# Kernel tuning notes

Measured on AMD Instinct MI355X. Metric: run time of the kernel, lower is better.

## Reference

```python
import jax, jax.numpy as jnp
import numpy as np

OUT_FEATURES = 11008
IN_FEATURES = 4096
BLOCK_SIZE = 128
NUM_BLOCKS = IN_FEATURES // BLOCK_SIZE  # 32
M_TOKENS = 4096  # flattened batch*seq


def _pack_int4(q):
    # q: int8 values in [-8, 7], flattened; pack 2 nibbles per int8 (matches pack_int4_to_int8)
    flat = q.reshape(-1)
    u = (flat.astype(jnp.int32) + 8).astype(jnp.uint8)
    packed = (u[0::2] | (u[1::2] << 4)).astype(jnp.int8)
    return packed


def _unpack_int4(packed, shape):
    # matches unpack_int8_to_int4
    pu = packed.astype(jnp.uint8)
    lower = pu & 15
    upper = (pu >> 4) & 15
    un = jnp.stack([lower, upper], axis=1).reshape(-1)
    n = int(np.prod(shape))
    un = un[:n].astype(jnp.int8) - 8
    return un.reshape(shape)


def setup_inputs() -> dict:
    key = jax.random.key(0)
    k_x, k_w, k_b = jax.random.split(key, 3)
    x = jax.random.normal(k_x, (M_TOKENS, IN_FEATURES), dtype=jnp.float32)
    w = jax.random.normal(k_w, (OUT_FEATURES, IN_FEATURES), dtype=jnp.float32) * 0.02
    bias = jax.random.normal(k_b, (OUT_FEATURES,), dtype=jnp.float32) * 0.01
    # blockwise symmetric 4-bit quantization (matches _quantize_blockwise)
    wr = w.reshape(OUT_FEATURES, NUM_BLOCKS, BLOCK_SIZE).transpose(1, 2, 0)  # (nb, bs, out)
    max_val = jnp.max(jnp.abs(wr), axis=1, keepdims=True)  # (nb, 1, out)
    qmax = 7.0
    scale3 = jnp.clip(max_val / qmax, 1e-8, None)
    q = jnp.clip(jnp.round(wr / scale3), -8, 7).astype(jnp.int8)  # (nb, bs, out)
    scale = scale3.squeeze(1)  # (nb, out)
    packed_w = _pack_int4(q)
    return {"x": x, "packed_w": packed_w, "scale": scale, "bias": bias}


def reference(x, packed_w, scale, bias):
    # unpack int4 nibbles -> (num_blocks, block_size, out)
    q = _unpack_int4(packed_w, (NUM_BLOCKS, BLOCK_SIZE, OUT_FEATURES))
    # dequantize with per-(block, out-channel) scale
    w_deq = q.astype(jnp.float32) * scale[:, None, :]  # (nb, bs, out)
    # y = x @ W^T + b, with x blocked along the in dimension
    xb = x.reshape(x.shape[0], NUM_BLOCKS, BLOCK_SIZE)
    y = jnp.einsum('mnb,nbo->mo', xb, w_deq) + bias
    return y
```

## Files before the change

### kernel.cpp

```cpp
#include <hip/hip_runtime.h>
#include <hip/hip_bf16.h>
#include <stdint.h>

#define NOUT 11008
#define KIN  4096
#define MTOK 4096
#define PLD  5504
#define NSTEP 128
#define NTN 43
#define NTM 16
#define ACHUNK 16384
#define BCHUNK 16384
#define WSA_BYTES ((size_t)NTM * NSTEP * ACHUNK)
#define WSW_BYTES ((size_t)NTN * NSTEP * BCHUNK)

typedef short bf16x8 __attribute__((ext_vector_type(8)));
typedef float f32x4  __attribute__((ext_vector_type(4)));

typedef __attribute__((address_space(3))) uint8_t lds_u8_t;
typedef __attribute__((address_space(1))) const uint8_t glb_u8_t;

__device__ __forceinline__ uint32_t bfpack(float lo, float hi){
    __hip_bfloat16 a = __float2bfloat16(lo);
    __hip_bfloat16 b = __float2bfloat16(hi);
    uint16_t ua, ub;
    __builtin_memcpy(&ua, &a, 2);
    __builtin_memcpy(&ub, &b, 2);
    return (uint32_t)ua | ((uint32_t)ub << 16);
}

__device__ __forceinline__ int swzA(int r){ return ((r >> 1) & 3) << 4; }

__global__ __launch_bounds__(256)
void prepA(const float* __restrict__ x, uint8_t* __restrict__ wsA)
{
    int gid = blockIdx.x * 256 + threadIdx.x;
    int m  = gid >> 10;
    int k  = (gid & 1023) << 2;
    float4 v = *reinterpret_cast<const float4*>(x + (size_t)m * KIN + k);
    uint32_t lo = bfpack(v.x, v.y), hi = bfpack(v.z, v.w);
    int mt = m >> 8, ml = m & 255, t = k >> 5, kl = k & 31;
    size_t dst = (size_t)(mt * NSTEP + t) * ACHUNK + ml * 64 + ((kl * 2) ^ swzA(ml));
    *reinterpret_cast<uint2*>(wsA + dst) = make_uint2(lo, hi);
}

__global__ __launch_bounds__(256)
void prepW2(const int32_t* __restrict__ pw, const float* __restrict__ sc,
            uint8_t* __restrict__ wsW)
{
    const int t  = blockIdx.x;
    const int nt = blockIdx.y;
    const int c  = threadIdx.x;
    const int col = nt * 256 + c;
    const int np  = col >> 1;
    const uint32_t sh = (uint32_t)(col & 1) * 4;
    const int32_t* p = pw + (size_t)(t * 32) * PLD + np;
    const float s  = sc[(size_t)(t >> 2) * NOUT + col];
    const float m8 = -8.f * s;
    uint8_t* out = wsW + ((size_t)nt * NSTEP + t) * BCHUNK + c * 64;
#pragma unroll
    for (int k8 = 0; k8 < 4; ++k8) {
        uint32_t r[4];
#pragma unroll
        for (int kk = 0; kk < 4; ++kk) {
            uint32_t w0 = (uint32_t)p[(size_t)(k8 * 8 + kk * 2)     * PLD];
            uint32_t w1 = (uint32_t)p[(size_t)(k8 * 8 + kk * 2 + 1) * PLD];
            float f0 = fmaf((float)((w0 >> sh) & 15u), s, m8);
            float f1 = fmaf((float)((w1 >> sh) & 15u), s, m8);
            r[kk] = bfpack(f0, f1);
        }
        *reinterpret_cast<uint4*>(out + ((k8 * 16) ^ swzA(c))) = *reinterpret_cast<uint4*>(r);
    }
}

__global__ __launch_bounds__(512, 1)
void qlin_gemm8(const uint8_t* __restrict__ wsA, const uint8_t* __restrict__ wsW,
                const float* __restrict__ bias, float* __restrict__ y)
{
    __shared__ __align__(16) uint8_t ldsA[4][ACHUNK];
    __shared__ __align__(16) uint8_t ldsB[4][BCHUNK];

    const int tid  = threadIdx.x;
    const int lane = tid & 63;
    const int wid  = tid >> 6;
    const int wr = wid >> 2, wc = wid & 3;

    const int lb = (blockIdx.x & 7) * 86 + (blockIdx.x >> 3);
    const int mt = lb / NTN, nt = lb % NTN;
    const int m0 = mt * 256, n0 = nt * 256;

    const int cl = lane & 15;
    const int k8 = lane >> 4;

    int aOff[8];
#pragma unroll
    for (int i = 0; i < 8; ++i) {
        int ml = wr * 128 + i * 16 + cl;
        aOff[i] = ml * 64 + ((k8 * 16) ^ swzA(ml));
    }
    int bOff[4];
#pragma unroll
    for (int j = 0; j < 4; ++j) {
        int cc = wc * 64 + j * 16 + cl;
        bOff[j] = cc * 64 + ((k8 * 16) ^ swzA(cc));
    }

    const uint8_t* wsAbase = wsA + (size_t)mt * NSTEP * ACHUNK;
    const uint8_t* wsWbase = wsW + (size_t)nt * NSTEP * BCHUNK;

    f32x4 acc[8][4];
#pragma unroll
    for (int i = 0; i < 8; ++i)
#pragma unroll
        for (int j = 0; j < 4; ++j)
            acc[i][j] = (f32x4){0.f, 0.f, 0.f, 0.f};

    bf16x8 af[4], bfr[4];

#define STAGE_A(buf, t) do { \
    const uint8_t* g_ = wsAbase + (size_t)(t) * ACHUNK + tid * 16; \
    __builtin_amdgcn_global_load_lds((glb_u8_t*)(g_),        (lds_u8_t*)(&ldsA[buf][tid*16]),        16, 0, 0); \
    __builtin_amdgcn_global_load_lds((glb_u8_t*)(g_ + 8192), (lds_u8_t*)(&ldsA[buf][tid*16 + 8192]), 16, 0, 0); \
} while(0)

#define STAGE_B(buf, t) do { \
    const uint8_t* g_ = wsWbase + (size_t)(t) * BCHUNK + tid * 16; \
    __builtin_amdgcn_global_load_lds((glb_u8_t*)(g_),        (lds_u8_t*)(&ldsB[buf][tid*16]),        16, 0, 0); \
    __builtin_amdgcn_global_load_lds((glb_u8_t*)(g_ + 8192), (lds_u8_t*)(&ldsB[buf][tid*16 + 8192]), 16, 0, 0); \
} while(0)

#define BAR() do { \
    asm volatile("" ::: "memory"); \
    __builtin_amdgcn_s_barrier(); \
    asm volatile("" ::: "memory"); \
} while(0)

#define PHASE_ODD(cb, sb, st) do { \
    STAGE_A(sb, st); \
    _Pragma("unroll") \
    for (int i = 0; i < 4; ++i) \
        af[i] = *reinterpret_cast<const bf16x8*>(ldsA[cb] + aOff[i]); \
    _Pragma("unroll") \
    for (int j = 0; j < 4; ++j) \
        bfr[j] = *reinterpret_cast<const bf16x8*>(ldsB[cb] + bOff[j]); \
    BAR(); \
    asm volatile("s_waitcnt lgkmcnt(0)" ::: "memory"); \
    __builtin_amdgcn_sched_barrier(0); \
    __builtin_amdgcn_s_setprio(1); \
    _Pragma("unroll") \
    for (int j = 0; j < 4; ++j) \
        _Pragma("unroll") \
        for (int i = 0; i < 4; ++i) \
            acc[i][j] = __builtin_amdgcn_mfma_f32_16x16x32_bf16(af[i], bfr[j], acc[i][j], 0, 0, 0); \
    __builtin_amdgcn_s_setprio(0); \
    BAR(); \
} while(0)

#define PHASE_EVEN(cb, sb, st) do { \
    STAGE_B(sb, st); \
    _Pragma("unroll") \
    for (int i = 0; i < 4; ++i) \
        af[i] = *reinterpret_cast<const bf16x8*>(ldsA[cb] + aOff[4 + i]); \
    BAR(); \
    asm volatile("s_waitcnt lgkmcnt(0)" ::: "memory"); \
    __builtin_amdgcn_sched_barrier(0); \
    __builtin_amdgcn_s_setprio(1); \
    _Pragma("unroll") \
    for (int j = 0; j < 4; ++j) \
        _Pragma("unroll") \
        for (int i = 0; i < 4; ++i) \
            acc[4 + i][j] = __builtin_amdgcn_mfma_f32_16x16x32_bf16(af[i], bfr[j], acc[4 + i][j], 0, 0, 0); \
    __builtin_amdgcn_s_setprio(0); \
    asm volatile("s_waitcnt vmcnt(8)" ::: "memory"); \
    __builtin_amdgcn_sched_barrier(0); \
    BAR(); \
} while(0)

    STAGE_A(0, 0); STAGE_B(0, 0);
    STAGE_A(1, 1); STAGE_B(1, 1);
    STAGE_A(2, 2); STAGE_B(2, 2);
    asm volatile("s_waitcnt vmcnt(8)" ::: "memory");
    __builtin_amdgcn_sched_barrier(0);
    BAR();

#pragma unroll 1
    for (int tb = 0; tb < NSTEP; tb += 4) {
        const int s4 = (tb + 4 < NSTEP) ? tb + 4 : NSTEP - 1;
        const int s5 = (tb + 5 < NSTEP) ? tb + 5 : NSTEP - 1;
        const int s6 = (tb + 6 < NSTEP) ? tb + 6 : NSTEP - 1;
        PHASE_ODD (0, 3, tb + 3);
        PHASE_EVEN(0, 3, tb + 3);
        PHASE_ODD (1, 0, s4);
        PHASE_EVEN(1, 0, s4);
        PHASE_ODD (2, 1, s5);
        PHASE_EVEN(2, 1, s5);
        PHASE_ODD (3, 2, s6);
        PHASE_EVEN(3, 2, s6);
    }

    float bv[4];
#pragma unroll
    for (int j = 0; j < 4; ++j) bv[j] = bias[n0 + wc * 64 + j * 16 + cl];
    const int rg = (lane >> 4) * 4;
#pragma unroll
    for (int i = 0; i < 8; ++i) {
        const int mrow = m0 + wr * 128 + i * 16 + rg;
#pragma unroll
        for (int r = 0; r < 4; ++r) {
            float* yp = y + (size_t)(mrow + r) * NOUT + n0 + wc * 64 + cl;
#pragma unroll
            for (int j = 0; j < 4; ++j)
                yp[j * 16] = acc[i][j][r] + bv[j];
        }
    }

#undef STAGE_A
#undef STAGE_B
#undef BAR
#undef PHASE_ODD
#undef PHASE_EVEN
}

extern "C" void kernel_launch(void* const* d_in, const int* in_sizes, int n_in,
                              void* d_out, int out_size, void* d_ws, size_t ws_size,
                              hipStream_t stream)
{
    const float*   xin  = (const float*)d_in[0];
    const int32_t* pw   = (const int32_t*)d_in[1];
    const float*   scal = (const float*)d_in[2];
    const float*   bias = (const float*)d_in[3];
    float* y = (float*)d_out;

    uint8_t* wsA = (uint8_t*)d_ws;
    uint8_t* wsW = wsA + WSA_BYTES;

    prepA<<<dim3((MTOK * (KIN / 4)) / 256), 256, 0, stream>>>(xin, wsA);
    prepW2<<<dim3(NSTEP, NTN), 256, 0, stream>>>(pw, scal, wsW);
    qlin_gemm8<<<dim3(NTM * NTN), 512, 0, stream>>>(wsA, wsW, bias, y);
}
```

Baseline: 411.2 us.

## Double-buffer MFMA register fragments and prefetch next tile's LDS reads

Restructures the GEMM main loop so the A and B fragments for the next K-step are read from LDS during the current step's second-half MFMAs. It ping-pongs between two B fragment register sets and uses partial lgkmcnt waits instead of draining all LDS reads. The global-load wait is tightened from vmcnt(8) to vmcnt(4) so the next LDS buffer is resident before it is read ahead. In exchange, fewer global-to-LDS stages stay in flight and register pressure rises from the extra fragment buffers.

After: 435.8 us. +6.0%, slower.

```diff
diff --git a/kernel.cpp b/kernel.cpp
--- a/kernel.cpp
+++ b/kernel.cpp
@@ -74,7 +74,7 @@
 }
 
 __global__ __launch_bounds__(512, 1)
-void qlin_gemm8(const uint8_t* __restrict__ wsA, const uint8_t* __restrict__ wsW,
+void qlin_gemm9(const uint8_t* __restrict__ wsA, const uint8_t* __restrict__ wsW,
                 const float* __restrict__ bias, float* __restrict__ y)
 {
     __shared__ __align__(16) uint8_t ldsA[4][ACHUNK];
@@ -92,9 +92,9 @@
     const int cl = lane & 15;
     const int k8 = lane >> 4;
 
-    int aOff[8];
-#pragma unroll
-    for (int i = 0; i < 8; ++i) {
+    int aOff[4];
+#pragma unroll
+    for (int i = 0; i < 4; ++i) {
         int ml = wr * 128 + i * 16 + cl;
         aOff[i] = ml * 64 + ((k8 * 16) ^ swzA(ml));
     }
@@ -115,7 +115,7 @@
         for (int j = 0; j < 4; ++j)
             acc[i][j] = (f32x4){0.f, 0.f, 0.f, 0.f};
 
-    bf16x8 af[4], bfr[4];
+    bf16x8 AF0[4], AF1[4], BF0[4], BF1[4];
 
 #define STAGE_A(buf, t) do { \
     const uint8_t* g_ = wsAbase + (size_t)(t) * ACHUNK + tid * 16; \
@@ -135,43 +135,47 @@
     asm volatile("" ::: "memory"); \
 } while(0)
 
-#define PHASE_ODD(cb, sb, st) do { \
+#define RD_AF0(cbn) do { _Pragma("unroll") \
+    for (int i = 0; i < 4; ++i) AF0[i] = *reinterpret_cast<const bf16x8*>(ldsA[cbn] + aOff[i]); } while(0)
+#define RD_AF1(cb) do { _Pragma("unroll") \
+    for (int i = 0; i < 4; ++i) AF1[i] = *reinterpret_cast<const bf16x8*>(ldsA[cb] + aOff[i] + 4096); } while(0)
+#define RD_BF0(cbn) do { _Pragma("unroll") \
+    for (int j = 0; j < 4; ++j) BF0[j] = *reinterpret_cast<const bf16x8*>(ldsB[cbn] + bOff[j]); } while(0)
+#define RD_BF1(cbn) do { _Pragma("unroll") \
+    for (int j = 0; j < 4; ++j) BF1[j] = *reinterpret_cast<const bf16x8*>(ldsB[cbn] + bOff[j]); } while(0)
+
+#define MFMA_H0(BFS) do { _Pragma("unroll") \
+    for (int j = 0; j < 4; ++j) { _Pragma("unroll") \
+        for (int i = 0; i < 4; ++i) \
+            acc[i][j] = __builtin_amdgcn_mfma_f32_16x16x32_bf16(AF0[i], BFS[j], acc[i][j], 0, 0, 0); } } while(0)
+#define MFMA_H1(BFS) do { _Pragma("unroll") \
+    for (int j = 0; j < 4; ++j) { _Pragma("unroll") \
+        for (int i = 0; i < 4; ++i) \
+            acc[4+i][j] = __builtin_amdgcn_mfma_f32_16x16x32_bf16(AF1[i], BFS[j], acc[4+i][j], 0, 0, 0); } } while(0)
+
+#define PH_O(cb, sb, st, BFC) do { \
     STAGE_A(sb, st); \
-    _Pragma("unroll") \
-    for (int i = 0; i < 4; ++i) \
-        af[i] = *reinterpret_cast<const bf16x8*>(ldsA[cb] + aOff[i]); \
-    _Pragma("unroll") \
-    for (int j = 0; j < 4; ++j) \
-        bfr[j] = *reinterpret_cast<const bf16x8*>(ldsB[cb] + bOff[j]); \
-    BAR(); \
-    asm volatile("s_waitcnt lgkmcnt(0)" ::: "memory"); \
+    RD_AF1(cb); \
+    BAR(); \
+    asm volatile("s_waitcnt lgkmcnt(4)" ::: "memory"); \
     __builtin_amdgcn_sched_barrier(0); \
     __builtin_amdgcn_s_setprio(1); \
-    _Pragma("unroll") \
-    for (int j = 0; j < 4; ++j) \
-        _Pragma("unroll") \
-        for (int i = 0; i < 4; ++i) \
-            acc[i][j] = __builtin_amdgcn_mfma_f32_16x16x32_bf16(af[i], bfr[j], acc[i][j], 0, 0, 0); \
+    MFMA_H0(BFC); \
     __builtin_amdgcn_s_setprio(0); \
     BAR(); \
 } while(0)
 
-#define PHASE_EVEN(cb, sb, st) do { \
+#define PH_E(cb, cbn, sb, st, BFC, RD_BFN) do { \
     STAGE_B(sb, st); \
-    _Pragma("unroll") \
-    for (int i = 0; i < 4; ++i) \
-        af[i] = *reinterpret_cast<const bf16x8*>(ldsA[cb] + aOff[4 + i]); \
-    BAR(); \
-    asm volatile("s_waitcnt lgkmcnt(0)" ::: "memory"); \
+    RD_AF0(cbn); \
+    RD_BFN(cbn); \
+    BAR(); \
+    asm volatile("s_waitcnt lgkmcnt(8)" ::: "memory"); \
     __builtin_amdgcn_sched_barrier(0); \
     __builtin_amdgcn_s_setprio(1); \
-    _Pragma("unroll") \
-    for (int j = 0; j < 4; ++j) \
-        _Pragma("unroll") \
-        for (int i = 0; i < 4; ++i) \
-            acc[4 + i][j] = __builtin_amdgcn_mfma_f32_16x16x32_bf16(af[i], bfr[j], acc[4 + i][j], 0, 0, 0); \
+    MFMA_H1(BFC); \
     __builtin_amdgcn_s_setprio(0); \
-    asm volatile("s_waitcnt vmcnt(8)" ::: "memory"); \
+    asm volatile("s_waitcnt vmcnt(4)" ::: "memory"); \
     __builtin_amdgcn_sched_barrier(0); \
     BAR(); \
 } while(0)
@@ -179,23 +183,21 @@
     STAGE_A(0, 0); STAGE_B(0, 0);
     STAGE_A(1, 1); STAGE_B(1, 1);
     STAGE_A(2, 2); STAGE_B(2, 2);
-    asm volatile("s_waitcnt vmcnt(8)" ::: "memory");
+    asm volatile("s_waitcnt vmcnt(4)" ::: "memory");
     __builtin_amdgcn_sched_barrier(0);
     BAR();
+    RD_AF0(0);
+    RD_BF0(0);
 
 #pragma unroll 1
     for (int tb = 0; tb < NSTEP; tb += 4) {
         const int s4 = (tb + 4 < NSTEP) ? tb + 4 : NSTEP - 1;
         const int s5 = (tb + 5 < NSTEP) ? tb + 5 : NSTEP - 1;
         const int s6 = (tb + 6 < NSTEP) ? tb + 6 : NSTEP - 1;
-        PHASE_ODD (0, 3, tb + 3);
-        PHASE_EVEN(0, 3, tb + 3);
-        PHASE_ODD (1, 0, s4);
-        PHASE_EVEN(1, 0, s4);
-        PHASE_ODD (2, 1, s5);
-        PHASE_EVEN(2, 1, s5);
-        PHASE_ODD (3, 2, s6);
-        PHASE_EVEN(3, 2, s6);
+        PH_O(0, 3, tb + 3, BF0);  PH_E(0, 1, 3, tb + 3, BF0, RD_BF1);
+        PH_O(1, 0, s4,     BF1);  PH_E(1, 2, 0, s4,     BF1, RD_BF0);
+        PH_O(2, 1, s5,     BF0);  PH_E(2, 3, 1, s5,     BF0, RD_BF1);
+        PH_O(3, 2, s6,     BF1);  PH_E(3, 0, 2, s6,     BF1, RD_BF0);
     }
 
     float bv[4];
@@ -217,8 +219,14 @@
 #undef STAGE_A
 #undef STAGE_B
 #undef BAR
-#undef PHASE_ODD
-#undef PHASE_EVEN
+#undef RD_AF0
+#undef RD_AF1
+#undef RD_BF0
+#undef RD_BF1
+#undef MFMA_H0
+#undef MFMA_H1
+#undef PH_O
+#undef PH_E
 }
 
 extern "C" void kernel_launch(void* const* d_in, const int* in_sizes, int n_in,
@@ -236,5 +244,5 @@
 
     prepA<<<dim3((MTOK * (KIN / 4)) / 256), 256, 0, stream>>>(xin, wsA);
     prepW2<<<dim3(NSTEP, NTN), 256, 0, stream>>>(pw, scal, wsW);
-    qlin_gemm8<<<dim3(NTM * NTN), 512, 0, stream>>>(wsA, wsW, bias, y);
-}
+    qlin_gemm9<<<dim3(NTM * NTN), 512, 0, stream>>>(wsA, wsW, bias, y);
+}
```

## Keep weights packed int4 in workspace and dequantize inside GEMM mainloop

Applied to the files above, without the earlier changes.

The weight prep kernel now repacks int4 nibbles into a compact byte layout plus per-column scales instead of writing fully dequantized bf16 tiles. The GEMM stages these smaller chunks into LDS and decodes B fragments in registers right before the MFMAs. This cuts workspace writes and the GEMM's global and LDS traffic for B. The cost is ALU work for decoding in the hot loop, and the B staging now uses 4-byte global-to-LDS loads, three per thread instead of two 16-byte loads.

Result: slower. 737.0 us (+79.2%).

```diff
diff --git a/kernel.cpp b/kernel.cpp
--- a/kernel.cpp
+++ b/kernel.cpp
@@ -10,9 +10,9 @@
 #define NTN 43
 #define NTM 16
 #define ACHUNK 16384
-#define BCHUNK 16384
+#define BCH    6144
 #define WSA_BYTES ((size_t)NTM * NSTEP * ACHUNK)
-#define WSW_BYTES ((size_t)NTN * NSTEP * BCHUNK)
+#define WSB_BYTES ((size_t)NTN * NSTEP * BCH)
 
 typedef short bf16x8 __attribute__((ext_vector_type(8)));
 typedef float f32x4  __attribute__((ext_vector_type(4)));
@@ -30,6 +30,24 @@
 }
 
 __device__ __forceinline__ int swzA(int r){ return ((r >> 1) & 3) << 4; }
+
+__device__ __forceinline__ bf16x8 decodeFrag(uint2 w, uint32_t sh, float s, float m8s)
+{
+    uint32_t a = (w.x >> sh) & 0x0f0f0f0fu;
+    uint32_t b = (w.y >> sh) & 0x0f0f0f0fu;
+    float d0 = fmaf((float)(a & 0xffu),         s, m8s);
+    float d1 = fmaf((float)((a >> 8) & 0xffu),  s, m8s);
+    float d2 = fmaf((float)((a >> 16) & 0xffu), s, m8s);
+    float d3 = fmaf((float)(a >> 24),           s, m8s);
+    float d4 = fmaf((float)(b & 0xffu),         s, m8s);
+    float d5 = fmaf((float)((b >> 8) & 0xffu),  s, m8s);
+    float d6 = fmaf((float)((b >> 16) & 0xffu), s, m8s);
+    float d7 = fmaf((float)(b >> 24),           s, m8s);
+    uint32_t r[4] = { bfpack(d0, d1), bfpack(d2, d3), bfpack(d4, d5), bfpack(d6, d7) };
+    bf16x8 out;
+    __builtin_memcpy(&out, r, 16);
+    return out;
+}
 
 __global__ __launch_bounds__(256)
 void prepA(const float* __restrict__ x, uint8_t* __restrict__ wsA)
@@ -45,40 +63,37 @@
 }
 
 __global__ __launch_bounds__(256)
-void prepW2(const int32_t* __restrict__ pw, const float* __restrict__ sc,
-            uint8_t* __restrict__ wsW)
+void prepB3(const int32_t* __restrict__ pw, const float* __restrict__ sc,
+            uint8_t* __restrict__ wsB)
 {
     const int t  = blockIdx.x;
     const int nt = blockIdx.y;
-    const int c  = threadIdx.x;
-    const int col = nt * 256 + c;
-    const int np  = col >> 1;
-    const uint32_t sh = (uint32_t)(col & 1) * 4;
-    const int32_t* p = pw + (size_t)(t * 32) * PLD + np;
-    const float s  = sc[(size_t)(t >> 2) * NOUT + col];
-    const float m8 = -8.f * s;
-    uint8_t* out = wsW + ((size_t)nt * NSTEP + t) * BCHUNK + c * 64;
-#pragma unroll
-    for (int k8 = 0; k8 < 4; ++k8) {
-        uint32_t r[4];
-#pragma unroll
-        for (int kk = 0; kk < 4; ++kk) {
-            uint32_t w0 = (uint32_t)p[(size_t)(k8 * 8 + kk * 2)     * PLD];
-            uint32_t w1 = (uint32_t)p[(size_t)(k8 * 8 + kk * 2 + 1) * PLD];
-            float f0 = fmaf((float)((w0 >> sh) & 15u), s, m8);
-            float f1 = fmaf((float)((w1 >> sh) & 15u), s, m8);
-            r[kk] = bfpack(f0, f1);
+    const int tid = threadIdx.x;
+    uint8_t* out = wsB + ((size_t)nt * NSTEP + t) * BCH;
+    if (tid < 128) {
+        const int np = tid;
+        const int32_t* p = pw + (size_t)(t * 32) * PLD + nt * 128 + np;
+#pragma unroll
+        for (int g = 0; g < 4; ++g) {
+            uint64_t v = 0;
+#pragma unroll
+            for (int i = 0; i < 8; ++i)
+                v |= (uint64_t)((uint32_t)p[(size_t)(g * 8 + i) * PLD] & 0xFFu) << (8 * i);
+            *reinterpret_cast<uint64_t*>(out + np * 32 + ((g * 8) ^ ((np & 3) * 8))) = v;
         }
-        *reinterpret_cast<uint4*>(out + ((k8 * 16) ^ swzA(c))) = *reinterpret_cast<uint4*>(r);
+    } else {
+        const int c2 = tid - 128;
+        float2 s = *reinterpret_cast<const float2*>(sc + (size_t)(t >> 2) * NOUT + nt * 256 + 2 * c2);
+        *reinterpret_cast<float2*>(out + 4096 + 8 * c2) = s;
     }
 }
 
 __global__ __launch_bounds__(512, 1)
-void qlin_gemm8(const uint8_t* __restrict__ wsA, const uint8_t* __restrict__ wsW,
-                const float* __restrict__ bias, float* __restrict__ y)
+void qlin_gemm11(const uint8_t* __restrict__ wsA, const uint8_t* __restrict__ wsB,
+                 const float* __restrict__ bias, float* __restrict__ y)
 {
     __shared__ __align__(16) uint8_t ldsA[4][ACHUNK];
-    __shared__ __align__(16) uint8_t ldsB[4][BCHUNK];
+    __shared__ __align__(16) uint8_t ldsB[4][BCH];
 
     const int tid  = threadIdx.x;
     const int lane = tid & 63;
@@ -91,6 +106,7 @@
 
     const int cl = lane & 15;
     const int k8 = lane >> 4;
+    const uint32_t sh4 = (uint32_t)(cl & 1) * 4;
 
     int aOff[8];
 #pragma unroll
@@ -98,15 +114,17 @@
         int ml = wr * 128 + i * 16 + cl;
         aOff[i] = ml * 64 + ((k8 * 16) ^ swzA(ml));
     }
-    int bOff[4];
+    int bpOff[4], scOff[4];
 #pragma unroll
     for (int j = 0; j < 4; ++j) {
-        int cc = wc * 64 + j * 16 + cl;
-        bOff[j] = cc * 64 + ((k8 * 16) ^ swzA(cc));
+        int col = wc * 64 + j * 16 + cl;
+        int np  = col >> 1;
+        bpOff[j] = np * 32 + ((k8 * 8) ^ ((np & 3) * 8));
+        scOff[j] = 4096 + col * 4;
     }
 
     const uint8_t* wsAbase = wsA + (size_t)mt * NSTEP * ACHUNK;
-    const uint8_t* wsWbase = wsW + (size_t)nt * NSTEP * BCHUNK;
+    const uint8_t* wsBbase = wsB + (size_t)nt * NSTEP * BCH;
 
     f32x4 acc[8][4];
 #pragma unroll
@@ -115,18 +133,19 @@
         for (int j = 0; j < 4; ++j)
             acc[i][j] = (f32x4){0.f, 0.f, 0.f, 0.f};
 
-    bf16x8 af[4], bfr[4];
+    bf16x8 AF[4], BF[4];
 
 #define STAGE_A(buf, t) do { \
-    const uint8_t* g_ = wsAbase + (size_t)(t) * ACHUNK + tid * 16; \
-    __builtin_amdgcn_global_load_lds((glb_u8_t*)(g_),        (lds_u8_t*)(&ldsA[buf][tid*16]),        16, 0, 0); \
-    __builtin_amdgcn_global_load_lds((glb_u8_t*)(g_ + 8192), (lds_u8_t*)(&ldsA[buf][tid*16 + 8192]), 16, 0, 0); \
+    const uint8_t* gA_ = wsAbase + (size_t)(t) * ACHUNK + tid * 16; \
+    __builtin_amdgcn_global_load_lds((glb_u8_t*)(gA_),        (lds_u8_t*)(&ldsA[buf][tid*16]),        16, 0, 0); \
+    __builtin_amdgcn_global_load_lds((glb_u8_t*)(gA_ + 8192), (lds_u8_t*)(&ldsA[buf][tid*16 + 8192]), 16, 0, 0); \
 } while(0)
 
 #define STAGE_B(buf, t) do { \
-    const uint8_t* g_ = wsWbase + (size_t)(t) * BCHUNK + tid * 16; \
-    __builtin_amdgcn_global_load_lds((glb_u8_t*)(g_),        (lds_u8_t*)(&ldsB[buf][tid*16]),        16, 0, 0); \
-    __builtin_amdgcn_global_load_lds((glb_u8_t*)(g_ + 8192), (lds_u8_t*)(&ldsB[buf][tid*16 + 8192]), 16, 0, 0); \
+    const uint8_t* gB_ = wsBbase + (size_t)(t) * BCH + tid * 4; \
+    __builtin_amdgcn_global_load_lds((glb_u8_t*)(gB_),        (lds_u8_t*)(&ldsB[buf][tid*4]),        4, 0, 0); \
+    __builtin_amdgcn_global_load_lds((glb_u8_t*)(gB_ + 2048), (lds_u8_t*)(&ldsB[buf][tid*4 + 2048]), 4, 0, 0); \
+    __builtin_amdgcn_global_load_lds((glb_u8_t*)(gB_ + 4096), (lds_u8_t*)(&ldsB[buf][tid*4 + 4096]), 4, 0, 0); \
 } while(0)
 
 #define BAR() do { \
@@ -135,43 +154,46 @@
     asm volatile("" ::: "memory"); \
 } while(0)
 
-#define PHASE_ODD(cb, sb, st) do { \
+#define PH_O(cb, sb, st) do { \
     STAGE_A(sb, st); \
-    _Pragma("unroll") \
-    for (int i = 0; i < 4; ++i) \
-        af[i] = *reinterpret_cast<const bf16x8*>(ldsA[cb] + aOff[i]); \
-    _Pragma("unroll") \
-    for (int j = 0; j < 4; ++j) \
-        bfr[j] = *reinterpret_cast<const bf16x8*>(ldsB[cb] + bOff[j]); \
-    BAR(); \
+    uint2 braw_[4]; float ss_[4]; \
+    _Pragma("unroll") \
+    for (int j = 0; j < 4; ++j) braw_[j] = *reinterpret_cast<const uint2*>(ldsB[cb] + bpOff[j]); \
+    _Pragma("unroll") \
+    for (int j = 0; j < 4; ++j) ss_[j] = *reinterpret_cast<const float*>(ldsB[cb] + scOff[j]); \
+    __builtin_amdgcn_sched_barrier(0); \
+    _Pragma("unroll") \
+    for (int i = 0; i < 4; ++i) AF[i] = *reinterpret_cast<const bf16x8*>(ldsA[cb] + aOff[i]); \
+    BAR(); \
+    asm volatile("s_waitcnt lgkmcnt(4)" ::: "memory"); \
+    __builtin_amdgcn_sched_barrier(0); \
+    _Pragma("unroll") \
+    for (int j = 0; j < 4; ++j) BF[j] = decodeFrag(braw_[j], sh4, ss_[j], -8.f * ss_[j]); \
     asm volatile("s_waitcnt lgkmcnt(0)" ::: "memory"); \
     __builtin_amdgcn_sched_barrier(0); \
     __builtin_amdgcn_s_setprio(1); \
     _Pragma("unroll") \
-    for (int j = 0; j < 4; ++j) \
-        _Pragma("unroll") \
+    for (int j = 0; j < 4; ++j) { _Pragma("unroll") \
         for (int i = 0; i < 4; ++i) \
-            acc[i][j] = __builtin_amdgcn_mfma_f32_16x16x32_bf16(af[i], bfr[j], acc[i][j], 0, 0, 0); \
+            acc[i][j] = __builtin_amdgcn_mfma_f32_16x16x32_bf16(AF[i], BF[j], acc[i][j], 0, 0, 0); } \
     __builtin_amdgcn_s_setprio(0); \
     BAR(); \
 } while(0)
 
-#define PHASE_EVEN(cb, sb, st) do { \
+#define PH_E(cb, sb, st) do { \
     STAGE_B(sb, st); \
     _Pragma("unroll") \
-    for (int i = 0; i < 4; ++i) \
-        af[i] = *reinterpret_cast<const bf16x8*>(ldsA[cb] + aOff[4 + i]); \
+    for (int i = 0; i < 4; ++i) AF[i] = *reinterpret_cast<const bf16x8*>(ldsA[cb] + aOff[4 + i]); \
     BAR(); \
     asm volatile("s_waitcnt lgkmcnt(0)" ::: "memory"); \
     __builtin_amdgcn_sched_barrier(0); \
     __builtin_amdgcn_s_setprio(1); \
     _Pragma("unroll") \
-    for (int j = 0; j < 4; ++j) \
-        _Pragma("unroll") \
+    for (int j = 0; j < 4; ++j) { _Pragma("unroll") \
         for (int i = 0; i < 4; ++i) \
-            acc[4 + i][j] = __builtin_amdgcn_mfma_f32_16x16x32_bf16(af[i], bfr[j], acc[4 + i][j], 0, 0, 0); \
+            acc[4 + i][j] = __builtin_amdgcn_mfma_f32_16x16x32_bf16(AF[i], BF[j], acc[4 + i][j], 0, 0, 0); } \
     __builtin_amdgcn_s_setprio(0); \
-    asm volatile("s_waitcnt vmcnt(8)" ::: "memory"); \
+    asm volatile("s_waitcnt vmcnt(10)" ::: "memory"); \
     __builtin_amdgcn_sched_barrier(0); \
     BAR(); \
 } while(0)
@@ -179,7 +201,7 @@
     STAGE_A(0, 0); STAGE_B(0, 0);
     STAGE_A(1, 1); STAGE_B(1, 1);
     STAGE_A(2, 2); STAGE_B(2, 2);
-    asm volatile("s_waitcnt vmcnt(8)" ::: "memory");
+    asm volatile("s_waitcnt vmcnt(10)" ::: "memory");
     __builtin_amdgcn_sched_barrier(0);
     BAR();
 
@@ -188,14 +210,10 @@
         const int s4 = (tb + 4 < NSTEP) ? tb + 4 : NSTEP - 1;
         const int s5 = (tb + 5 < NSTEP) ? tb + 5 : NSTEP - 1;
         const int s6 = (tb + 6 < NSTEP) ? tb + 6 : NSTEP - 1;
-        PHASE_ODD (0, 3, tb + 3);
-        PHASE_EVEN(0, 3, tb + 3);
-        PHASE_ODD (1, 0, s4);
-        PHASE_EVEN(1, 0, s4);
-        PHASE_ODD (2, 1, s5);
-        PHASE_EVEN(2, 1, s5);
-        PHASE_ODD (3, 2, s6);
-        PHASE_EVEN(3, 2, s6);
+        PH_O(0, 3, tb + 3);  PH_E(0, 3, tb + 3);
+        PH_O(1, 0, s4);      PH_E(1, 0, s4);
+        PH_O(2, 1, s5);      PH_E(2, 1, s5);
+        PH_O(3, 2, s6);      PH_E(3, 2, s6);
     }
 
     float bv[4];
@@ -217,8 +235,8 @@
 #undef STAGE_A
 #undef STAGE_B
 #undef BAR
-#undef PHASE_ODD
-#undef PHASE_EVEN
+#undef PH_O
+#undef PH_E
 }
 
 extern "C" void kernel_launch(void* const* d_in, const int* in_sizes, int n_in,
@@ -232,9 +250,9 @@
     float* y = (float*)d_out;
 
     uint8_t* wsA = (uint8_t*)d_ws;
-    uint8_t* wsW = wsA + WSA_BYTES;
+    uint8_t* wsB = wsA + WSA_BYTES;
 
     prepA<<<dim3((MTOK * (KIN / 4)) / 256), 256, 0, stream>>>(xin, wsA);
-    prepW2<<<dim3(NSTEP, NTN), 256, 0, stream>>>(pw, scal, wsW);
-    qlin_gemm8<<<dim3(NTM * NTN), 512, 0, stream>>>(wsA, wsW, bias, y);
-}
+    prepB3<<<dim3(NSTEP, NTN), 256, 0, stream>>>(pw, scal, wsB);
+    qlin_gemm11<<<dim3(NTM * NTN), 512, 0, stream>>>(wsA, wsB, bias, y);
+}
```
